# Optimization experiments

Hardware: AMD Instinct MI355X
Metric: run time of the kernel (lower is better)

## Reference

```python
import jax, jax.numpy as jnp
import numpy as np

NUM_HEADS = 8
NUM_POINTS = 9


def _bilinear_sample(img, gx, gy):
    """grid_sample, mode=bilinear, padding=zeros, align_corners=True.
    img: (B, C, H, W); gx, gy: (B, M) pixel coords. Returns (B, C, M)."""
    Bc, C, H, W = img.shape
    imgf = img.reshape(Bc, C, H * W)
    x0 = jnp.floor(gx)
    y0 = jnp.floor(gy)
    wx1 = gx - x0
    wy1 = gy - y0

    def corner(xi, yi, w):
        valid = (xi >= 0) & (xi < W) & (yi >= 0) & (yi < H)
        xi_c = jnp.clip(xi, 0, W - 1).astype(jnp.int32)
        yi_c = jnp.clip(yi, 0, H - 1).astype(jnp.int32)
        idx = yi_c * W + xi_c  # (B, M)
        g = jax.vmap(lambda im, ix: im[:, ix])(imgf, idx)  # (B, C, M)
        return g * (w * valid)[:, None, :]

    return (corner(x0, y0, (1 - wx1) * (1 - wy1))
            + corner(x0 + 1, y0, wx1 * (1 - wy1))
            + corner(x0, y0 + 1, (1 - wx1) * wy1)
            + corner(x0 + 1, y0 + 1, wx1 * wy1))


def setup_inputs() -> dict:
    key = jax.random.key(0)
    ks = jax.random.split(key, 6)
    B, Hp, Wp, T, D = 4, 64, 64, 3, 256
    N = Hp * Wp
    Hh, P = NUM_HEADS, NUM_POINTS
    x = jax.random.normal(ks[0], (B, N, T, D), dtype=jnp.float32)
    # offset/attn projections: small random (orig inits them to 0, which is degenerate for testing)
    W_off = jax.random.normal(ks[1], (D, Hh * P * 2), dtype=jnp.float32) * 0.01
    b_off = jnp.zeros((Hh * P * 2,), dtype=jnp.float32)
    W_attn = jax.random.normal(ks[2], (D, Hh * P), dtype=jnp.float32) * 0.01
    b_attn = jnp.zeros((Hh * P,), dtype=jnp.float32)
    W_v = jax.random.normal(ks[3], (D, D), dtype=jnp.float32) * 0.02
    b_v = jnp.zeros((D,), dtype=jnp.float32)
    W_o = jax.random.normal(ks[4], (D, D), dtype=jnp.float32) * 0.02
    b_o = jnp.zeros((D,), dtype=jnp.float32)
    return {"x": x, "W_off": W_off, "b_off": b_off, "W_attn": W_attn,
            "b_attn": b_attn, "W_v": W_v, "b_v": b_v, "W_o": W_o,
            "b_o": b_o, "Hp": Hp, "Wp": Wp}


def reference(x, W_off, b_off, W_attn, b_attn, W_v, b_v, W_o, b_o, Hp, Wp):
    B, N, T, D = x.shape
    Hh, P = NUM_HEADS, NUM_POINTS
    dh = D // Hh

    query = x[:, :, T // 2]  # (B, N, D) middle frame
    offset = (query @ W_off + b_off).reshape(B, N, Hh, P, 2)
    attn = jax.nn.softmax((query @ W_attn + b_attn).reshape(B, N, Hh, P), axis=-1)

    # reference points in [-1, 1], xy order (x = width coord)
    gh, gw = jnp.meshgrid(jnp.arange(Hp, dtype=jnp.float32),
                          jnp.arange(Wp, dtype=jnp.float32), indexing='ij')
    ref = jnp.stack([gw, gh], axis=-1).reshape(N, 2)
    ref = ref / jnp.asarray([Wp - 1, Hp - 1], dtype=jnp.float32) * 2 - 1

    loc = ref[None, :, None, None, :] + offset  # (B, N, H, P, 2) normalized

    value = (x @ W_v + b_v).reshape(B, N, T, Hh, dh)
    # (B, H, T, dh, N) -> (B*H*T, dh, Hp, Wp)
    val = jnp.transpose(value, (0, 3, 2, 4, 1)).reshape(B * Hh * T, dh, Hp, Wp)

    # per-(b,h) grid, shared across frames; fold T into batch of the sampler
    grid = jnp.transpose(loc, (0, 2, 1, 3, 4))  # (B, H, N, P, 2)
    grid = jnp.broadcast_to(grid[:, :, None], (B, Hh, T, N, P, 2))
    grid = grid.reshape(B * Hh * T, N * P, 2)
    gx = (grid[..., 0] + 1) * 0.5 * (Wp - 1)
    gy = (grid[..., 1] + 1) * 0.5 * (Hp - 1)

    sampled = _bilinear_sample(val, gx, gy)  # (B*H*T, dh, N*P)
    sampled = sampled.reshape(B, Hh, T, dh, N, P)

    # weighted sum over points, summed over frames
    out = jnp.einsum('bhtdnp,bnhp->bnhd', sampled, attn).reshape(B, N, D)
    return out @ W_o + b_o
```

## Files before the change

kernel.cpp:

```cpp
#include <hip/hip_runtime.h>
#include <hip/hip_bf16.h>


#define NH_ 8
#define DH_ 32
#define MM_ 16384

typedef __attribute__((ext_vector_type(8))) short bf16x8;
typedef __attribute__((ext_vector_type(4))) short bf16x4;
typedef __attribute__((ext_vector_type(4))) float f32x4;

static __device__ __forceinline__ unsigned short f2bf(float f) {
  unsigned int u = __float_as_uint(f);
  u = (u + 0x7fff + ((u >> 16) & 1)) >> 16;
  return (unsigned short)u;
}
static __device__ __forceinline__ float bf2f(unsigned short h) {
  return __uint_as_float(((unsigned int)h) << 16);
}

__global__ __launch_bounds__(256) void prep_w(
    const float* __restrict__ W_off, const float* __restrict__ W_attn,
    const float* __restrict__ W_v, const float* __restrict__ W_o,
    const float* __restrict__ b_off, const float* __restrict__ b_attn,
    unsigned short* __restrict__ wvh, unsigned short* __restrict__ wvl,
    unsigned short* __restrict__ wch, unsigned short* __restrict__ wcl,
    unsigned short* __restrict__ woh, unsigned short* __restrict__ wol,
    float* __restrict__ bcat) {
  const int n = blockIdx.x, t = threadIdx.x;
  {
    float v = W_v[(size_t)t * 256 + n];
    unsigned short h = f2bf(v);
    wvh[n * 256 + t] = h; wvl[n * 256 + t] = f2bf(v - bf2f(h));
  }
  {
    float v = W_o[(size_t)t * 256 + n];
    unsigned short h = f2bf(v);
    woh[n * 256 + t] = h; wol[n * 256 + t] = f2bf(v - bf2f(h));
  }
  if (n < 216) {
    float v = (n < 144) ? W_off[(size_t)t * 144 + n] : W_attn[(size_t)t * 72 + (n - 144)];
    unsigned short h = f2bf(v);
    wch[n * 256 + t] = h; wcl[n * 256 + t] = f2bf(v - bf2f(h));
  }
  if (n == 0 && t < 216) bcat[t] = (t < 144) ? b_off[t] : b_attn[t - 144];
}

__global__ __launch_bounds__(256) void prep_a(const float* __restrict__ x,
                                              unsigned short* __restrict__ ash,
                                              unsigned short* __restrict__ asl) {
  const int gid = blockIdx.x * 256 + threadIdx.x;
  const int row = gid >> 6, c4 = (gid & 63) * 4;
  const float* xr = x + (size_t)row * 768 + c4;
  float4 a0 = *(const float4*)xr;
  float4 a1 = *(const float4*)(xr + 256);
  float4 a2 = *(const float4*)(xr + 512);
  float s[4] = {a0.x + a1.x + a2.x, a0.y + a1.y + a2.y,
                a0.z + a1.z + a2.z, a0.w + a1.w + a2.w};
  bf16x4 hv, lv;
#pragma unroll
  for (int j = 0; j < 4; ++j) {
    unsigned short h = f2bf(s[j]);
    hv[j] = (short)h;
    lv[j] = (short)f2bf(s[j] - bf2f(h));
  }
  *(bf16x4*)(ash + (size_t)row * 256 + c4) = hv;
  *(bf16x4*)(asl + (size_t)row * 256 + c4) = lv;
}

__global__ __launch_bounds__(256) void mgemm01(
    const unsigned short* __restrict__ Ahi, const unsigned short* __restrict__ Alo,
    const float* __restrict__ X,
    const unsigned short* __restrict__ Wvh, const unsigned short* __restrict__ Wvl,
    const unsigned short* __restrict__ Wch, const unsigned short* __restrict__ Wcl,
    const float* __restrict__ b_v, const float* __restrict__ bcat,
    float* __restrict__ valsum, float* __restrict__ proj) {
  __shared__ unsigned short Ah[64][64], Al[64][64], Bh[128][64], Bl[128][64];
  const int mode1 = (blockIdx.y >= 2);
  const int n0 = (blockIdx.y & 1) * 128;
  const int m0 = blockIdx.x * 64;
  const int tid = threadIdx.x;
  const int wid = tid >> 6, lane = tid & 63;
  const int am = (wid >> 1) * 32, bn = (wid & 1) * 64;
  const int fr = lane & 15, kg = lane >> 4;
  const unsigned short* Bth = mode1 ? Wch : Wvh;
  const unsigned short* Btl = mode1 ? Wcl : Wvl;

  f32x4 acc[2][4];
#pragma unroll
  for (int i = 0; i < 2; ++i)
#pragma unroll
    for (int j = 0; j < 4; ++j) acc[i][j] = (f32x4)(0.f);

  for (int k0 = 0; k0 < 256; k0 += 64) {
#pragma unroll
    for (int i = 0; i < 2; ++i) {
      int cid = i * 256 + tid;
      int r = cid >> 3, c = cid & 7;
      int dst = r * 64 + ((c ^ (r & 7)) * 8);
      bf16x8 hv, lv;
      if (mode1) {
        const float* src = X + ((size_t)(m0 + r) * 3 + 1) * 256 + k0 + c * 8;
        float4 f0 = *(const float4*)src, f1 = *(const float4*)(src + 4);
        float vv[8] = {f0.x, f0.y, f0.z, f0.w, f1.x, f1.y, f1.z, f1.w};
#pragma unroll
        for (int j = 0; j < 8; ++j) {
          unsigned short h = f2bf(vv[j]);
          hv[j] = (short)h;
          lv[j] = (short)f2bf(vv[j] - bf2f(h));
        }
      } else {
        size_t off = (size_t)(m0 + r) * 256 + k0 + c * 8;
        hv = *(const bf16x8*)(Ahi + off);
        lv = *(const bf16x8*)(Alo + off);
      }
      *(bf16x8*)(&Ah[0][0] + dst) = hv;
      *(bf16x8*)(&Al[0][0] + dst) = lv;
    }
#pragma unroll
    for (int i = 0; i < 4; ++i) {
      int cid = i * 256 + tid;
      int r = cid >> 3, c = cid & 7;
      int dst = r * 64 + ((c ^ (r & 7)) * 8);
      int nrow = n0 + r;
      bf16x8 hv = (bf16x8)(short)0, lv = (bf16x8)(short)0;
      if (!mode1 || nrow < 216) {
        size_t off = (size_t)nrow * 256 + k0 + c * 8;
        hv = *(const bf16x8*)(Bth + off);
        lv = *(const bf16x8*)(Btl + off);
      }
      *(bf16x8*)(&Bh[0][0] + dst) = hv;
      *(bf16x8*)(&Bl[0][0] + dst) = lv;
    }
    __syncthreads();

#pragma unroll
    for (int ks = 0; ks < 2; ++ks) {
      const int kc = ks * 4 + kg;
      bf16x8 ah[2], al[2], bh[4], bl[4];
#pragma unroll
      for (int mi = 0; mi < 2; ++mi) {
        int m = am + mi * 16 + fr;
        int o = m * 64 + ((kc ^ (m & 7)) * 8);
        ah[mi] = *(const bf16x8*)(&Ah[0][0] + o);
        al[mi] = *(const bf16x8*)(&Al[0][0] + o);
      }
#pragma unroll
      for (int ni = 0; ni < 4; ++ni) {
        int n = bn + ni * 16 + fr;
        int o = n * 64 + ((kc ^ (n & 7)) * 8);
        bh[ni] = *(const bf16x8*)(&Bh[0][0] + o);
        bl[ni] = *(const bf16x8*)(&Bl[0][0] + o);
      }
#pragma unroll
      for (int mi = 0; mi < 2; ++mi)
#pragma unroll
        for (int ni = 0; ni < 4; ++ni) {
          acc[mi][ni] = __builtin_amdgcn_mfma_f32_16x16x32_bf16(ah[mi], bh[ni], acc[mi][ni], 0, 0, 0);
          acc[mi][ni] = __builtin_amdgcn_mfma_f32_16x16x32_bf16(ah[mi], bl[ni], acc[mi][ni], 0, 0, 0);
          acc[mi][ni] = __builtin_amdgcn_mfma_f32_16x16x32_bf16(al[mi], bh[ni], acc[mi][ni], 0, 0, 0);
        }
    }
    __syncthreads();
  }

  const int ro = kg * 4;
#pragma unroll
  for (int mi = 0; mi < 2; ++mi)
#pragma unroll
    for (int ni = 0; ni < 4; ++ni) {
      int col = n0 + bn + ni * 16 + fr;
      if (mode1 && col >= 216) continue;
      int rowb = m0 + am + mi * 16 + ro;
      float bv = mode1 ? bcat[col] : b_v[col] * 3.f;
#pragma unroll
      for (int r = 0; r < 4; ++r) {
        int grow = rowb + r;
        float v = acc[mi][ni][r] + bv;
        if (mode1) {
          proj[(size_t)grow * 216 + col] = v;
        } else {
          int b = grow >> 12, nn = grow & 4095;
          int h = col >> 5, d = col & 31;
          valsum[(((size_t)(b * NH_ + h) << 12) + nn) * DH_ + d] = v;
        }
      }
    }
}

__global__ __launch_bounds__(256) void mgemm2(
    const unsigned short* __restrict__ Ahi, const unsigned short* __restrict__ Alo,
    const unsigned short* __restrict__ Bth, const unsigned short* __restrict__ Btl,
    const float* __restrict__ bias, float* __restrict__ Cout) {
  __shared__ unsigned short Ah[64][64], Al[64][64], Bh[128][64], Bl[128][64];
  const int n0 = blockIdx.y * 128;
  const int m0 = blockIdx.x * 64;
  const int tid = threadIdx.x;
  const int wid = tid >> 6, lane = tid & 63;
  const int am = (wid >> 1) * 32, bn = (wid & 1) * 64;
  const int fr = lane & 15, kg = lane >> 4;

  f32x4 acc[2][4];
#pragma unroll
  for (int i = 0; i < 2; ++i)
#pragma unroll
    for (int j = 0; j < 4; ++j) acc[i][j] = (f32x4)(0.f);

  for (int k0 = 0; k0 < 256; k0 += 64) {
#pragma unroll
    for (int i = 0; i < 2; ++i) {
      int cid = i * 256 + tid;
      int r = cid >> 3, c = cid & 7;
      int dst = r * 64 + ((c ^ (r & 7)) * 8);
      size_t off = (size_t)(m0 + r) * 256 + k0 + c * 8;
      *(bf16x8*)(&Ah[0][0] + dst) = *(const bf16x8*)(Ahi + off);
      *(bf16x8*)(&Al[0][0] + dst) = *(const bf16x8*)(Alo + off);
    }
#pragma unroll
    for (int i = 0; i < 4; ++i) {
      int cid = i * 256 + tid;
      int r = cid >> 3, c = cid & 7;
      int dst = r * 64 + ((c ^ (r & 7)) * 8);
      size_t off = (size_t)(n0 + r) * 256 + k0 + c * 8;
      *(bf16x8*)(&Bh[0][0] + dst) = *(const bf16x8*)(Bth + off);
      *(bf16x8*)(&Bl[0][0] + dst) = *(const bf16x8*)(Btl + off);
    }
    __syncthreads();

#pragma unroll
    for (int ks = 0; ks < 2; ++ks) {
      const int kc = ks * 4 + kg;
      bf16x8 ah[2], al[2], bh[4], bl[4];
#pragma unroll
      for (int mi = 0; mi < 2; ++mi) {
        int m = am + mi * 16 + fr;
        int o = m * 64 + ((kc ^ (m & 7)) * 8);
        ah[mi] = *(const bf16x8*)(&Ah[0][0] + o);
        al[mi] = *(const bf16x8*)(&Al[0][0] + o);
      }
#pragma unroll
      for (int ni = 0; ni < 4; ++ni) {
        int n = bn + ni * 16 + fr;
        int o = n * 64 + ((kc ^ (n & 7)) * 8);
        bh[ni] = *(const bf16x8*)(&Bh[0][0] + o);
        bl[ni] = *(const bf16x8*)(&Bl[0][0] + o);
      }
#pragma unroll
      for (int mi = 0; mi < 2; ++mi)
#pragma unroll
        for (int ni = 0; ni < 4; ++ni) {
          acc[mi][ni] = __builtin_amdgcn_mfma_f32_16x16x32_bf16(ah[mi], bh[ni], acc[mi][ni], 0, 0, 0);
          acc[mi][ni] = __builtin_amdgcn_mfma_f32_16x16x32_bf16(ah[mi], bl[ni], acc[mi][ni], 0, 0, 0);
          acc[mi][ni] = __builtin_amdgcn_mfma_f32_16x16x32_bf16(al[mi], bh[ni], acc[mi][ni], 0, 0, 0);
        }
    }
    __syncthreads();
  }

  const int ro = kg * 4;
#pragma unroll
  for (int mi = 0; mi < 2; ++mi)
#pragma unroll
    for (int ni = 0; ni < 4; ++ni) {
      int col = n0 + bn + ni * 16 + fr;
      int rowb = m0 + am + mi * 16 + ro;
      float bv = bias[col];
#pragma unroll
      for (int r = 0; r < 4; ++r)
        Cout[(size_t)(rowb + r) * 256 + col] = acc[mi][ni][r] + bv;
    }
}

__global__ __launch_bounds__(64) void sample_k(const float* __restrict__ valsum,
                                               const float* __restrict__ proj,
                                               unsigned short* __restrict__ ihi,
                                               unsigned short* __restrict__ ilo) {
  const int bid = blockIdx.x;
  const int row = ((bid & 7) << 11) + (bid >> 3);
  const int b = row >> 12, n = row & 4095;

  __shared__ int cidx[72][4];
  __shared__ float cw[72][4];
  __shared__ float sa[72];

  const int t = threadIdx.x;
  const float* pr = proj + (size_t)row * 216;
  for (int e = t; e < 72; e += 64) {
    float ox = pr[e * 2], oy = pr[e * 2 + 1];
    float gx = (float)(n & 63) + ox * 31.5f;
    float gy = (float)(n >> 6) + oy * 31.5f;
    float fx0 = floorf(gx), fy0 = floorf(gy);
    float wx1 = gx - fx0, wy1 = gy - fy0;
    float wx0 = 1.f - wx1, wy0 = 1.f - wy1;
    int x0 = (int)fx0, y0 = (int)fy0, x1 = x0 + 1, y1 = y0 + 1;
    bool vx0 = (x0 >= 0) & (x0 < 64), vx1 = (x1 >= 0) & (x1 < 64);
    bool vy0 = (y0 >= 0) & (y0 < 64), vy1 = (y1 >= 0) & (y1 < 64);
    int x0c = min(max(x0, 0), 63), x1c = min(max(x1, 0), 63);
    int y0c = min(max(y0, 0), 63), y1c = min(max(y1, 0), 63);
    cidx[e][0] = (y0c * 64 + x0c) * DH_; cw[e][0] = (vx0 & vy0) ? wx0 * wy0 : 0.f;
    cidx[e][1] = (y0c * 64 + x1c) * DH_; cw[e][1] = (vx1 & vy0) ? wx1 * wy0 : 0.f;
    cidx[e][2] = (y1c * 64 + x0c) * DH_; cw[e][2] = (vx0 & vy1) ? wx0 * wy1 : 0.f;
    cidx[e][3] = (y1c * 64 + x1c) * DH_; cw[e][3] = (vx1 & vy1) ? wx1 * wy1 : 0.f;
  }
  if (t < 8) {
    const float* pa = pr + 144 + t * 9;
    float lg[9], mx = -1e30f;
#pragma unroll
    for (int p = 0; p < 9; ++p) { lg[p] = pa[p]; mx = fmaxf(mx, lg[p]); }
    float s = 0.f;
#pragma unroll
    for (int p = 0; p < 9; ++p) { lg[p] = __expf(lg[p] - mx); s += lg[p]; }
    float inv = 1.f / s;
#pragma unroll
    for (int p = 0; p < 9; ++p) sa[t * 9 + p] = lg[p] * inv;
  }
  __syncthreads();

  const int h = t >> 3, d4 = (t & 7) * 4;
  const float* vb = valsum + ((size_t)((b * NH_ + h) << 12)) * DH_ + d4;
  float ax = 0.f, ay = 0.f, az = 0.f, aw = 0.f;
#pragma unroll
  for (int p = 0; p < 9; ++p) {
    const int hp = h * 9 + p;
    float sx = 0.f, sy = 0.f, sz = 0.f, sw = 0.f;
#pragma unroll
    for (int c = 0; c < 4; ++c) {
      float4 v = *(const float4*)(vb + cidx[hp][c]);
      float w = cw[hp][c];
      sx += w * v.x; sy += w * v.y; sz += w * v.z; sw += w * v.w;
    }
    float ap = sa[hp];
    ax += ap * sx; ay += ap * sy; az += ap * sz; aw += ap * sw;
  }
  float av[4] = {ax, ay, az, aw};
  bf16x4 hv, lv;
#pragma unroll
  for (int j = 0; j < 4; ++j) {
    unsigned short hh = f2bf(av[j]);
    hv[j] = (short)hh;
    lv[j] = (short)f2bf(av[j] - bf2f(hh));
  }
  const size_t o = (size_t)row * 256 + t * 4;
  *(bf16x4*)(ihi + o) = hv;
  *(bf16x4*)(ilo + o) = lv;
}

extern "C" void kernel_launch(void* const* d_in, const int* in_sizes, int n_in,
                              void* d_out, int out_size, void* d_ws, size_t ws_size,
                              hipStream_t stream) {
  const float* x      = (const float*)d_in[0];
  const float* W_off  = (const float*)d_in[1];
  const float* b_off  = (const float*)d_in[2];
  const float* W_attn = (const float*)d_in[3];
  const float* b_attn = (const float*)d_in[4];
  const float* W_v    = (const float*)d_in[5];
  const float* b_v    = (const float*)d_in[6];
  const float* W_o    = (const float*)d_in[7];
  const float* b_o    = (const float*)d_in[8];
  float* out = (float*)d_out;

  float* valsum = (float*)d_ws;
  float* proj   = valsum + (size_t)MM_ * 256;
  float* bcat   = proj + (size_t)MM_ * 216;
  unsigned short* ash = (unsigned short*)(bcat + 256);
  unsigned short* asl = ash + (size_t)MM_ * 256;
  unsigned short* wvh = asl + (size_t)MM_ * 256;
  unsigned short* wvl = wvh + 65536;
  unsigned short* wch = wvl + 65536;
  unsigned short* wcl = wch + 55296;
  unsigned short* woh = wcl + 55296;
  unsigned short* wol = woh + 65536;
  unsigned short* ihi = ash;
  unsigned short* ilo = asl;

  prep_w<<<dim3(256), dim3(256), 0, stream>>>(W_off, W_attn, W_v, W_o, b_off, b_attn,
                                              wvh, wvl, wch, wcl, woh, wol, bcat);
  prep_a<<<dim3(MM_ / 4), dim3(256), 0, stream>>>(x, ash, asl);
  mgemm01<<<dim3(256, 4), dim3(256), 0, stream>>>(ash, asl, x, wvh, wvl, wch, wcl,
                                                  b_v, bcat, valsum, proj);
  sample_k<<<dim3(MM_), dim3(64), 0, stream>>>(valsum, proj, ihi, ilo);
  mgemm2<<<dim3(256, 2), dim3(256), 0, stream>>>(ihi, ilo, woh, wol, b_o, out);
}
```

Before: 176.5 us.

## Merge prep kernels, precompute middle-frame split bf16, pack four rows per sample block

The weight-prep and activation-prep kernels become one launch. That launch now also writes hi/lo bf16 splits of the middle frame, so the projection GEMM loads bf16 tiles directly instead of converting fp32 inside its load loop. The sampling kernel now handles four rows per 256-thread block instead of one row per 64-thread block, which reduces block count and scheduling overhead. The cost is an extra 16 MB of workspace writes and reads for the middle-frame split.

```diff
diff --git a/kernel.cpp b/kernel.cpp
--- a/kernel.cpp
+++ b/kernel.cpp
@@ -19,58 +19,63 @@
   return __uint_as_float(((unsigned int)h) << 16);
 }
 
-__global__ __launch_bounds__(256) void prep_w(
+__global__ __launch_bounds__(256) void prep(
+    const float* __restrict__ x,
     const float* __restrict__ W_off, const float* __restrict__ W_attn,
     const float* __restrict__ W_v, const float* __restrict__ W_o,
     const float* __restrict__ b_off, const float* __restrict__ b_attn,
+    unsigned short* __restrict__ ash, unsigned short* __restrict__ asl,
+    unsigned short* __restrict__ xmh, unsigned short* __restrict__ xml,
     unsigned short* __restrict__ wvh, unsigned short* __restrict__ wvl,
     unsigned short* __restrict__ wch, unsigned short* __restrict__ wcl,
     unsigned short* __restrict__ woh, unsigned short* __restrict__ wol,
     float* __restrict__ bcat) {
-  const int n = blockIdx.x, t = threadIdx.x;
-  {
-    float v = W_v[(size_t)t * 256 + n];
-    unsigned short h = f2bf(v);
-    wvh[n * 256 + t] = h; wvl[n * 256 + t] = f2bf(v - bf2f(h));
-  }
-  {
-    float v = W_o[(size_t)t * 256 + n];
-    unsigned short h = f2bf(v);
-    woh[n * 256 + t] = h; wol[n * 256 + t] = f2bf(v - bf2f(h));
-  }
-  if (n < 216) {
-    float v = (n < 144) ? W_off[(size_t)t * 144 + n] : W_attn[(size_t)t * 72 + (n - 144)];
-    unsigned short h = f2bf(v);
-    wch[n * 256 + t] = h; wcl[n * 256 + t] = f2bf(v - bf2f(h));
-  }
-  if (n == 0 && t < 216) bcat[t] = (t < 144) ? b_off[t] : b_attn[t - 144];
-}
-
-__global__ __launch_bounds__(256) void prep_a(const float* __restrict__ x,
-                                              unsigned short* __restrict__ ash,
-                                              unsigned short* __restrict__ asl) {
-  const int gid = blockIdx.x * 256 + threadIdx.x;
-  const int row = gid >> 6, c4 = (gid & 63) * 4;
-  const float* xr = x + (size_t)row * 768 + c4;
-  float4 a0 = *(const float4*)xr;
-  float4 a1 = *(const float4*)(xr + 256);
-  float4 a2 = *(const float4*)(xr + 512);
-  float s[4] = {a0.x + a1.x + a2.x, a0.y + a1.y + a2.y,
-                a0.z + a1.z + a2.z, a0.w + a1.w + a2.w};
-  bf16x4 hv, lv;
-#pragma unroll
-  for (int j = 0; j < 4; ++j) {
-    unsigned short h = f2bf(s[j]);
-    hv[j] = (short)h;
-    lv[j] = (short)f2bf(s[j] - bf2f(h));
-  }
-  *(bf16x4*)(ash + (size_t)row * 256 + c4) = hv;
-  *(bf16x4*)(asl + (size_t)row * 256 + c4) = lv;
+  const int bid = blockIdx.x, t = threadIdx.x;
+  if (bid < 4096) {
+    const int gid = bid * 256 + t;
+    const int row = gid >> 6, c4 = (gid & 63) * 4;
+    const float* xr = x + (size_t)row * 768 + c4;
+    float4 a0 = *(const float4*)xr;
+    float4 a1 = *(const float4*)(xr + 256);
+    float4 a2 = *(const float4*)(xr + 512);
+    float s[4] = {a0.x + a1.x + a2.x, a0.y + a1.y + a2.y,
+                  a0.z + a1.z + a2.z, a0.w + a1.w + a2.w};
+    float m[4] = {a1.x, a1.y, a1.z, a1.w};
+    bf16x4 shv, slv, mhv, mlv;
+#pragma unroll
+    for (int j = 0; j < 4; ++j) {
+      unsigned short h = f2bf(s[j]);
+      shv[j] = (short)h; slv[j] = (short)f2bf(s[j] - bf2f(h));
+      unsigned short h2 = f2bf(m[j]);
+      mhv[j] = (short)h2; mlv[j] = (short)f2bf(m[j] - bf2f(h2));
+    }
+    const size_t o = (size_t)row * 256 + c4;
+    *(bf16x4*)(ash + o) = shv;  *(bf16x4*)(asl + o) = slv;
+    *(bf16x4*)(xmh + o) = mhv;  *(bf16x4*)(xml + o) = mlv;
+  } else {
+    const int n = bid - 4096;
+    {
+      float v = W_v[(size_t)t * 256 + n];
+      unsigned short h = f2bf(v);
+      wvh[n * 256 + t] = h; wvl[n * 256 + t] = f2bf(v - bf2f(h));
+    }
+    {
+      float v = W_o[(size_t)t * 256 + n];
+      unsigned short h = f2bf(v);
+      woh[n * 256 + t] = h; wol[n * 256 + t] = f2bf(v - bf2f(h));
+    }
+    if (n < 216) {
+      float v = (n < 144) ? W_off[(size_t)t * 144 + n] : W_attn[(size_t)t * 72 + (n - 144)];
+      unsigned short h = f2bf(v);
+      wch[n * 256 + t] = h; wcl[n * 256 + t] = f2bf(v - bf2f(h));
+    }
+    if (n == 0 && t < 216) bcat[t] = (t < 144) ? b_off[t] : b_attn[t - 144];
+  }
 }
 
 __global__ __launch_bounds__(256) void mgemm01(
     const unsigned short* __restrict__ Ahi, const unsigned short* __restrict__ Alo,
-    const float* __restrict__ X,
+    const unsigned short* __restrict__ Xmh, const unsigned short* __restrict__ Xml,
     const unsigned short* __restrict__ Wvh, const unsigned short* __restrict__ Wvl,
     const unsigned short* __restrict__ Wch, const unsigned short* __restrict__ Wcl,
     const float* __restrict__ b_v, const float* __restrict__ bcat,
@@ -83,6 +88,8 @@
   const int wid = tid >> 6, lane = tid & 63;
   const int am = (wid >> 1) * 32, bn = (wid & 1) * 64;
   const int fr = lane & 15, kg = lane >> 4;
+  const unsigned short* Asrch = mode1 ? Xmh : Ahi;
+  const unsigned short* Asrcl = mode1 ? Xml : Alo;
   const unsigned short* Bth = mode1 ? Wch : Wvh;
   const unsigned short* Btl = mode1 ? Wcl : Wvl;
 
@@ -98,24 +105,9 @@
       int cid = i * 256 + tid;
       int r = cid >> 3, c = cid & 7;
       int dst = r * 64 + ((c ^ (r & 7)) * 8);
-      bf16x8 hv, lv;
-      if (mode1) {
-        const float* src = X + ((size_t)(m0 + r) * 3 + 1) * 256 + k0 + c * 8;
-        float4 f0 = *(const float4*)src, f1 = *(const float4*)(src + 4);
-        float vv[8] = {f0.x, f0.y, f0.z, f0.w, f1.x, f1.y, f1.z, f1.w};
-#pragma unroll
-        for (int j = 0; j < 8; ++j) {
-          unsigned short h = f2bf(vv[j]);
-          hv[j] = (short)h;
-          lv[j] = (short)f2bf(vv[j] - bf2f(h));
-        }
-      } else {
-        size_t off = (size_t)(m0 + r) * 256 + k0 + c * 8;
-        hv = *(const bf16x8*)(Ahi + off);
-        lv = *(const bf16x8*)(Alo + off);
-      }
-      *(bf16x8*)(&Ah[0][0] + dst) = hv;
-      *(bf16x8*)(&Al[0][0] + dst) = lv;
+      size_t off = (size_t)(m0 + r) * 256 + k0 + c * 8;
+      *(bf16x8*)(&Ah[0][0] + dst) = *(const bf16x8*)(Asrch + off);
+      *(bf16x8*)(&Al[0][0] + dst) = *(const bf16x8*)(Asrcl + off);
     }
 #pragma unroll
     for (int i = 0; i < 4; ++i) {
@@ -271,21 +263,22 @@
     }
 }
 
-__global__ __launch_bounds__(64) void sample_k(const float* __restrict__ valsum,
+__global__ __launch_bounds__(256) void sample4(const float* __restrict__ valsum,
                                                const float* __restrict__ proj,
                                                unsigned short* __restrict__ ihi,
                                                unsigned short* __restrict__ ilo) {
   const int bid = blockIdx.x;
-  const int row = ((bid & 7) << 11) + (bid >> 3);
+  const int wv = threadIdx.x >> 6;
+  const int lane = threadIdx.x & 63;
+  const int row = ((bid & 7) << 11) + ((bid >> 3) << 2) + wv;
   const int b = row >> 12, n = row & 4095;
 
-  __shared__ int cidx[72][4];
-  __shared__ float cw[72][4];
-  __shared__ float sa[72];
-
-  const int t = threadIdx.x;
+  __shared__ int cidx[4][72][4];
+  __shared__ float cw[4][72][4];
+  __shared__ float sa[4][72];
+
   const float* pr = proj + (size_t)row * 216;
-  for (int e = t; e < 72; e += 64) {
+  for (int e = lane; e < 72; e += 64) {
     float ox = pr[e * 2], oy = pr[e * 2 + 1];
     float gx = (float)(n & 63) + ox * 31.5f;
     float gy = (float)(n >> 6) + oy * 31.5f;
@@ -297,13 +290,13 @@
     bool vy0 = (y0 >= 0) & (y0 < 64), vy1 = (y1 >= 0) & (y1 < 64);
     int x0c = min(max(x0, 0), 63), x1c = min(max(x1, 0), 63);
     int y0c = min(max(y0, 0), 63), y1c = min(max(y1, 0), 63);
-    cidx[e][0] = (y0c * 64 + x0c) * DH_; cw[e][0] = (vx0 & vy0) ? wx0 * wy0 : 0.f;
-    cidx[e][1] = (y0c * 64 + x1c) * DH_; cw[e][1] = (vx1 & vy0) ? wx1 * wy0 : 0.f;
-    cidx[e][2] = (y1c * 64 + x0c) * DH_; cw[e][2] = (vx0 & vy1) ? wx0 * wy1 : 0.f;
-    cidx[e][3] = (y1c * 64 + x1c) * DH_; cw[e][3] = (vx1 & vy1) ? wx1 * wy1 : 0.f;
-  }
-  if (t < 8) {
-    const float* pa = pr + 144 + t * 9;
+    cidx[wv][e][0] = (y0c * 64 + x0c) * DH_; cw[wv][e][0] = (vx0 & vy0) ? wx0 * wy0 : 0.f;
+    cidx[wv][e][1] = (y0c * 64 + x1c) * DH_; cw[wv][e][1] = (vx1 & vy0) ? wx1 * wy0 : 0.f;
+    cidx[wv][e][2] = (y1c * 64 + x0c) * DH_; cw[wv][e][2] = (vx0 & vy1) ? wx0 * wy1 : 0.f;
+    cidx[wv][e][3] = (y1c * 64 + x1c) * DH_; cw[wv][e][3] = (vx1 & vy1) ? wx1 * wy1 : 0.f;
+  }
+  if (lane < 8) {
+    const float* pa = pr + 144 + lane * 9;
     float lg[9], mx = -1e30f;
 #pragma unroll
     for (int p = 0; p < 9; ++p) { lg[p] = pa[p]; mx = fmaxf(mx, lg[p]); }
@@ -312,11 +305,11 @@
     for (int p = 0; p < 9; ++p) { lg[p] = __expf(lg[p] - mx); s += lg[p]; }
     float inv = 1.f / s;
 #pragma unroll
-    for (int p = 0; p < 9; ++p) sa[t * 9 + p] = lg[p] * inv;
+    for (int p = 0; p < 9; ++p) sa[wv][lane * 9 + p] = lg[p] * inv;
   }
   __syncthreads();
 
-  const int h = t >> 3, d4 = (t & 7) * 4;
+  const int h = lane >> 3, d4 = (lane & 7) * 4;
   const float* vb = valsum + ((size_t)((b * NH_ + h) << 12)) * DH_ + d4;
   float ax = 0.f, ay = 0.f, az = 0.f, aw = 0.f;
 #pragma unroll
@@ -325,11 +318,11 @@
     float sx = 0.f, sy = 0.f, sz = 0.f, sw = 0.f;
 #pragma unroll
     for (int c = 0; c < 4; ++c) {
-      float4 v = *(const float4*)(vb + cidx[hp][c]);
-      float w = cw[hp][c];
+      float4 v = *(const float4*)(vb + cidx[wv][hp][c]);
+      float w = cw[wv][hp][c];
       sx += w * v.x; sy += w * v.y; sz += w * v.z; sw += w * v.w;
     }
-    float ap = sa[hp];
+    float ap = sa[wv][hp];
     ax += ap * sx; ay += ap * sy; az += ap * sz; aw += ap * sw;
   }
   float av[4] = {ax, ay, az, aw};
@@ -340,7 +333,7 @@
     hv[j] = (short)hh;
     lv[j] = (short)f2bf(av[j] - bf2f(hh));
   }
-  const size_t o = (size_t)row * 256 + t * 4;
+  const size_t o = (size_t)row * 256 + lane * 4;
   *(bf16x4*)(ihi + o) = hv;
   *(bf16x4*)(ilo + o) = lv;
 }
@@ -364,7 +357,9 @@
   float* bcat   = proj + (size_t)MM_ * 216;
   unsigned short* ash = (unsigned short*)(bcat + 256);
   unsigned short* asl = ash + (size_t)MM_ * 256;
-  unsigned short* wvh = asl + (size_t)MM_ * 256;
+  unsigned short* xmh = asl + (size_t)MM_ * 256;
+  unsigned short* xml = xmh + (size_t)MM_ * 256;
+  unsigned short* wvh = xml + (size_t)MM_ * 256;
   unsigned short* wvl = wvh + 65536;
   unsigned short* wch = wvl + 65536;
   unsigned short* wcl = wch + 55296;
@@ -373,11 +368,11 @@
   unsigned short* ihi = ash;
   unsigned short* ilo = asl;
 
-  prep_w<<<dim3(256), dim3(256), 0, stream>>>(W_off, W_attn, W_v, W_o, b_off, b_attn,
-                                              wvh, wvl, wch, wcl, woh, wol, bcat);
-  prep_a<<<dim3(MM_ / 4), dim3(256), 0, stream>>>(x, ash, asl);
-  mgemm01<<<dim3(256, 4), dim3(256), 0, stream>>>(ash, asl, x, wvh, wvl, wch, wcl,
+  prep<<<dim3(4352), dim3(256), 0, stream>>>(x, W_off, W_attn, W_v, W_o, b_off, b_attn,
+                                             ash, asl, xmh, xml,
+                                             wvh, wvl, wch, wcl, woh, wol, bcat);
+  mgemm01<<<dim3(256, 4), dim3(256), 0, stream>>>(ash, asl, xmh, xml, wvh, wvl, wch, wcl,
                                                   b_v, bcat, valsum, proj);
-  sample_k<<<dim3(MM_), dim3(64), 0, stream>>>(valsum, proj, ihi, ilo);
+  sample4<<<dim3(4096), dim3(256), 0, stream>>>(valsum, proj, ihi, ilo);
   mgemm2<<<dim3(256, 2), dim3(256), 0, stream>>>(ihi, ilo, woh, wol, b_o, out);
 }
```

After: 174.5 us. Within noise of the previous version (-1.1%).
